# Performance work log

Measured on AMD Instinct MI355X. Metric: run time of the kernel, lower is better.

The kernel has to match this reference:

```python
import jax, jax.numpy as jnp
import numpy as np

B, S, D, H = 2, 2048, 1024, 16
DH = D // H
CBS, STRIDE = 32, 16      # compress block size / sliding stride
NSEL = 16                 # num_selected_blocks
WIN = 16                  # sliding_window_size (half-width)
SCALE = DH ** -0.5


def setup_inputs() -> dict:
    key = jax.random.key(0)
    ks = jax.random.split(key, 12)
    s = 0.02
    return {
        "x": jax.random.normal(ks[0], (B, S, D), jnp.float32),
        "qkv_w": jax.random.normal(ks[1], (D, 3 * D), jnp.float32) * s,
        "qkv_b": jnp.zeros((3 * D,), jnp.float32),
        "c1_w": jax.random.normal(ks[2], (CBS * D, D), jnp.float32) * s,
        "c1_b": jnp.zeros((D,), jnp.float32),
        "c2_w": jax.random.normal(ks[3], (D, D), jnp.float32) * s,
        "c2_b": jnp.zeros((D,), jnp.float32),
        "score_w": jax.random.normal(ks[4], (D, 1), jnp.float32) * s,
        "score_b": jnp.zeros((1,), jnp.float32),
        "out_w": jax.random.normal(ks[5], (D, D), jnp.float32) * s,
        "out_b": jnp.zeros((D,), jnp.float32),
    }


def reference(x, qkv_w, qkv_b, c1_w, c1_b, c2_w, c2_b, score_w, score_b, out_w, out_b):
    # q, k, v: [B, H, S, DH]
    qkv = (x @ qkv_w + qkv_b).reshape(B, S, 3, H, DH).transpose(2, 0, 3, 1, 4)
    q, k, v = qkv[0], qkv[1], qkv[2]

    # --- token compression: overlapping blocks -> MLP ---
    starts = jnp.arange(0, S - CBS + 1, STRIDE)                 # [nb]
    blk_idx = starts[:, None] + jnp.arange(CBS)[None, :]        # [nb, CBS]
    blocks = x[:, blk_idx, :].reshape(B, starts.shape[0], CBS * D)
    hidden = jax.nn.relu(blocks @ c1_w + c1_b)
    compressed = hidden @ c2_w + c2_b                           # [B, nb, D]

    # --- block selection via learned scores + top-k ---
    scores = (compressed @ score_w + score_b)[..., 0]           # [B, nb]
    _, top_idx = jax.lax.top_k(scores, NSEL)                    # [B, NSEL]
    selected = jnp.take_along_axis(compressed, top_idx[:, :, None], axis=1)  # [B, NSEL, D]

    sqkv = (selected @ qkv_w + qkv_b).reshape(B, NSEL, 3, H, DH).transpose(2, 0, 3, 1, 4)
    sel_k, sel_v = sqkv[1], sqkv[2]                             # [B, H, NSEL, DH]

    # --- sliding-window local attention (vectorized gather of banded K/V) ---
    offs = jnp.arange(-WIN, WIN + 1)                            # [2W+1]
    pos = jnp.arange(S)[:, None] + offs[None, :]                # [S, 2W+1]
    valid = (pos >= 0) & (pos < S)
    pos_c = jnp.clip(pos, 0, S - 1)
    kw = k[:, :, pos_c, :]                                      # [B, H, S, 2W+1, DH]
    vw = v[:, :, pos_c, :]
    sc = jnp.einsum('bhsd,bhswd->bhsw', q, kw) * SCALE
    sc = jnp.where(valid[None, None], sc, -jnp.inf)
    local = jnp.einsum('bhsw,bhswd->bhsd', jax.nn.softmax(sc, axis=-1), vw)

    # --- global attention over selected compressed blocks ---
    gsc = jnp.einsum('bhsd,bhkd->bhsk', q, sel_k) * SCALE       # [B, H, S, NSEL]
    glob = jnp.einsum('bhsk,bhkd->bhsd', jax.nn.softmax(gsc, axis=-1), sel_v)

    out = (local + glob).transpose(0, 2, 1, 3).reshape(B, S, D)
    return out @ out_w + out_b
```

## Files before the change

### kernel.cpp

```cpp
#include <hip/hip_runtime.h>
#include <math.h>

#define BB   2
#define SS   2048
#define DD   1024
#define HH   16
#define DH   64
#define CBS  32
#define STRIDEC 16
#define NBLK 127
#define NSEL 16
#define WIN  16
#define NW   33
#define SCALE 0.125f
#define MC   254

typedef _Float16 f16;
typedef __attribute__((ext_vector_type(8))) _Float16 f16x8;
typedef __attribute__((ext_vector_type(4))) _Float16 f16x4;
typedef __attribute__((ext_vector_type(2))) _Float16 h2;
typedef __attribute__((ext_vector_type(4))) float f32x4;

__global__ __launch_bounds__(256) void convert_f16(
    const float* __restrict__ src, f16* __restrict__ dst, int n)
{
    const int i = (blockIdx.x * 256 + threadIdx.x) * 4;
    if (i >= n) return;
    float4 v = *(const float4*)(src + i);
    f16x4 o;
    o[0] = (f16)v.x; o[1] = (f16)v.y; o[2] = (f16)v.z; o[3] = (f16)v.w;
    *(f16x4*)(dst + i) = o;
}

__global__ __launch_bounds__(256) void transpose_conv(
    const float* __restrict__ src, f16* __restrict__ dst, int K, int N)
{
    __shared__ float t[32][33];
    const int n0 = blockIdx.x * 32, k0 = blockIdx.y * 32;
    const int tx = threadIdx.x & 31, ty = threadIdx.x >> 5;
#pragma unroll
    for (int r = 0; r < 32; r += 8)
        t[ty + r][tx] = src[(size_t)(k0 + ty + r) * N + n0 + tx];
    __syncthreads();
#pragma unroll
    for (int r = 0; r < 32; r += 8)
        dst[(size_t)(n0 + ty + r) * K + k0 + tx] = (f16)t[tx][ty + r];
}

__global__ __launch_bounds__(256) void gemm_f16(
    const f16* __restrict__ A, const f16* __restrict__ Bt,
    const float* __restrict__ bias, float* __restrict__ C,
    int M, int N, int K)
{
    constexpr int BK = 64;
    __shared__ f16 As[128 * BK];
    __shared__ f16 Bs[128 * BK];
    const int tid  = threadIdx.x;
    const int wid  = tid >> 6, lane = tid & 63;
    const int bm = blockIdx.y * 128, bn = blockIdx.x * 128;
    const int wm = (wid >> 1) * 64, wn = (wid & 1) * 64;

    const int lrow = lane >> 3;
    const int lk8  = (lane & 7) * 8;

    f32x4 acc[4][4];
#pragma unroll
    for (int i = 0; i < 4; ++i)
#pragma unroll
        for (int j = 0; j < 4; ++j) acc[i][j] = (f32x4){0.f, 0.f, 0.f, 0.f};

    for (int kt = 0; kt < K; kt += BK) {
#pragma unroll
        for (int c = 0; c < 4; ++c) {
            const int seg = c * 4 + wid;
            const int row = seg * 8 + lrow;
            const f16* ga = A + (size_t)(bm + row) * K + kt + lk8;
            __builtin_amdgcn_global_load_lds(
                (const __attribute__((address_space(1))) void*)(const void*)ga,
                (__attribute__((address_space(3))) void*)(void*)(As + seg * 512),
                16, 0, 0);
            const f16* gb = Bt + (size_t)(bn + row) * K + kt + lk8;
            __builtin_amdgcn_global_load_lds(
                (const __attribute__((address_space(1))) void*)(const void*)gb,
                (__attribute__((address_space(3))) void*)(void*)(Bs + seg * 512),
                16, 0, 0);
        }
        __syncthreads();

#pragma unroll
        for (int kk = 0; kk < 2; ++kk) {
            const int ko = kk * 32 + (lane >> 4) * 8;
            f16x8 a[4], b[4];
#pragma unroll
            for (int i = 0; i < 4; ++i)
                a[i] = *(const f16x8*)(As + (wm + i * 16 + (lane & 15)) * BK + ko);
#pragma unroll
            for (int j = 0; j < 4; ++j)
                b[j] = *(const f16x8*)(Bs + (wn + j * 16 + (lane & 15)) * BK + ko);
#pragma unroll
            for (int i = 0; i < 4; ++i)
#pragma unroll
                for (int j = 0; j < 4; ++j)
                    acc[i][j] = __builtin_amdgcn_mfma_f32_16x16x32_f16(
                        a[i], b[j], acc[i][j], 0, 0, 0);
        }
        __syncthreads();
    }

    const int rr0 = (lane >> 4) * 4;
    const int cc  = lane & 15;
#pragma unroll
    for (int i = 0; i < 4; ++i) {
        const int r = bm + wm + i * 16 + rr0;
#pragma unroll
        for (int j = 0; j < 4; ++j) {
            const int cn = bn + wn + j * 16 + cc;
            const float bv = bias[cn];
#pragma unroll
            for (int q = 0; q < 4; ++q)
                C[(size_t)(r + q) * N + cn] = acc[i][j][q] + bv;
        }
    }
}

#define C1_NZ 16
#define C1_KCHUNK 2048

__global__ __launch_bounds__(256) void gemm_c1(
    const f16* __restrict__ xh, const f16* __restrict__ Wt,
    float* __restrict__ P)
{
    constexpr int BK = 64;
    __shared__ f16 As[128 * BK];
    __shared__ f16 Bs[64 * BK];
    const int tid  = threadIdx.x;
    const int wid  = tid >> 6, lane = tid & 63;
    const int bn = blockIdx.x * 64, bm = blockIdx.y * 128;
    const int z  = blockIdx.z;
    const int wm = (wid >> 1) * 64, wn = (wid & 1) * 32;

    const int lrow = lane >> 3;
    const int lk8  = (lane & 7) * 8;

    f32x4 acc[4][2];
#pragma unroll
    for (int i = 0; i < 4; ++i)
#pragma unroll
        for (int j = 0; j < 2; ++j) acc[i][j] = (f32x4){0.f, 0.f, 0.f, 0.f};

    for (int t = 0; t < C1_KCHUNK / BK; ++t) {
        const int ktg = z * C1_KCHUNK + t * BK;
        const int kc  = (ktg + lk8) >> 10;
        const int kd  = (ktg + lk8) & 1023;
#pragma unroll
        for (int c = 0; c < 4; ++c) {
            const int seg = c * 4 + wid;
            int row = bm + seg * 8 + lrow;
            if (row > MC - 1) row = MC - 1;
            const int b   = (row >= NBLK) ? 1 : 0;
            const int blk = row - b * NBLK;
            const f16* ga = xh + ((size_t)(b * SS + blk * STRIDEC + kc) << 10) + kd;
            __builtin_amdgcn_global_load_lds(
                (const __attribute__((address_space(1))) void*)(const void*)ga,
                (__attribute__((address_space(3))) void*)(void*)(As + seg * 512),
                16, 0, 0);
        }
#pragma unroll
        for (int c = 0; c < 2; ++c) {
            const int seg = wid * 2 + c;
            const int row = bn + seg * 8 + lrow;
            const f16* gb = Wt + (size_t)row * (CBS * DD) + ktg + lk8;
            __builtin_amdgcn_global_load_lds(
                (const __attribute__((address_space(1))) void*)(const void*)gb,
                (__attribute__((address_space(3))) void*)(void*)(Bs + seg * 512),
                16, 0, 0);
        }
        __syncthreads();

#pragma unroll
        for (int kk = 0; kk < 2; ++kk) {
            const int ko = kk * 32 + (lane >> 4) * 8;
            f16x8 a[4], b[2];
#pragma unroll
            for (int i = 0; i < 4; ++i)
                a[i] = *(const f16x8*)(As + (wm + i * 16 + (lane & 15)) * BK + ko);
#pragma unroll
            for (int j = 0; j < 2; ++j)
                b[j] = *(const f16x8*)(Bs + (wn + j * 16 + (lane & 15)) * BK + ko);
#pragma unroll
            for (int i = 0; i < 4; ++i)
#pragma unroll
                for (int j = 0; j < 2; ++j)
                    acc[i][j] = __builtin_amdgcn_mfma_f32_16x16x32_f16(
                        a[i], b[j], acc[i][j], 0, 0, 0);
        }
        __syncthreads();
    }

    const int rr0 = (lane >> 4) * 4;
    const int cc  = lane & 15;
#pragma unroll
    for (int i = 0; i < 4; ++i) {
        const int r = bm + wm + i * 16 + rr0;
#pragma unroll
        for (int j = 0; j < 2; ++j) {
            const int cn = bn + wn + j * 16 + cc;
#pragma unroll
            for (int q = 0; q < 4; ++q)
                if (r + q < MC)
                    P[((size_t)z * MC + r + q) * DD + cn] = acc[i][j][q];
        }
    }
}

template<int MODE>
__global__ __launch_bounds__(256) void gemm128(
    const float* __restrict__ A, const float* __restrict__ Bm,
    const float* __restrict__ bias, float* __restrict__ C,
    int M, int N, int K, const int* __restrict__ selIdx, int flags)
{
    __shared__ float As[8][132];
    __shared__ float Bs[8][132];

    const int tid = threadIdx.x;
    const int bm = blockIdx.y * 128;
    const int bn = blockIdx.x * 128;
    const int nz = gridDim.z;
    const int z  = blockIdx.z;
    const int kchunk = K / nz;
    const int k0 = z * kchunk;
    const int kend = k0 + kchunk;

    const int tx = tid & 15;
    const int ty = tid >> 4;

    const int arow = tid >> 1;
    const int akq  = (tid & 1) * 4;
    const int bkr  = tid >> 5;
    const int bcol = (tid & 31) * 4;

    float acc[2][2][4][4];
#pragma unroll
    for (int qi = 0; qi < 2; ++qi)
#pragma unroll
        for (int qj = 0; qj < 2; ++qj)
#pragma unroll
            for (int i = 0; i < 4; ++i)
#pragma unroll
                for (int j = 0; j < 4; ++j) acc[qi][qj][i][j] = 0.f;

    auto loadA = [&](int kt) -> float4 {
        float4 av = make_float4(0.f, 0.f, 0.f, 0.f);
        const int grow = bm + arow;
        if (grow < M) {
            if constexpr (MODE == 0) {
                av = *(const float4*)(A + (size_t)grow * K + kt + akq);
            } else {
                const int b = grow >> 4;
                const int j = grow & 15;
                const int idx = selIdx[b * NSEL + j];
                av = *(const float4*)(A + (size_t)(b * NBLK + idx) * K + kt + akq);
            }
        }
        return av;
    };
    auto loadB = [&](int kt) -> float4 {
        return *(const float4*)(Bm + (size_t)(kt + bkr) * N + bn + bcol);
    };

    float4 av = loadA(k0);
    float4 bv = loadB(k0);

    for (int kt = k0; kt < kend; kt += 8) {
        As[akq + 0][arow] = av.x;
        As[akq + 1][arow] = av.y;
        As[akq + 2][arow] = av.z;
        As[akq + 3][arow] = av.w;
        *(float4*)&Bs[bkr][bcol] = bv;
        __syncthreads();
        if (kt + 8 < kend) {
            av = loadA(kt + 8);
            bv = loadB(kt + 8);
        }
#pragma unroll
        for (int k = 0; k < 8; ++k) {
            const float4 a0 = *(const float4*)&As[k][ty * 4];
            const float4 a1 = *(const float4*)&As[k][64 + ty * 4];
            const float4 b0 = *(const float4*)&Bs[k][tx * 4];
            const float4 b1 = *(const float4*)&Bs[k][64 + tx * 4];
            const float ar[2][4] = {{a0.x, a0.y, a0.z, a0.w},
                                    {a1.x, a1.y, a1.z, a1.w}};
            const float br[2][4] = {{b0.x, b0.y, b0.z, b0.w},
                                    {b1.x, b1.y, b1.z, b1.w}};
#pragma unroll
            for (int qi = 0; qi < 2; ++qi)
#pragma unroll
                for (int i = 0; i < 4; ++i)
#pragma unroll
                    for (int qj = 0; qj < 2; ++qj)
#pragma unroll
                        for (int j = 0; j < 4; ++j)
                            acc[qi][qj][i][j] += ar[qi][i] * br[qj][j];
        }
        __syncthreads();
    }

    if (nz == 1) {
        const bool hasB   = (flags & 1) != 0;
        const bool doRelu = (flags & 2) != 0;
#pragma unroll
        for (int qi = 0; qi < 2; ++qi)
#pragma unroll
            for (int i = 0; i < 4; ++i) {
                const int r = bm + qi * 64 + ty * 4 + i;
                if (r >= M) continue;
#pragma unroll
                for (int qj = 0; qj < 2; ++qj)
#pragma unroll
                    for (int j = 0; j < 4; ++j) {
                        const int cn = bn + qj * 64 + tx * 4 + j;
                        float v = acc[qi][qj][i][j];
                        if (hasB) v += bias[cn];
                        if (doRelu) v = fmaxf(v, 0.f);
                        C[(size_t)r * N + cn] = v;
                    }
            }
    } else {
        float* P = C + (size_t)z * M * N;
#pragma unroll
        for (int qi = 0; qi < 2; ++qi)
#pragma unroll
            for (int i = 0; i < 4; ++i) {
                const int r = bm + qi * 64 + ty * 4 + i;
                if (r >= M) continue;
#pragma unroll
                for (int qj = 0; qj < 2; ++qj)
#pragma unroll
                    for (int j = 0; j < 4; ++j) {
                        const int cn = bn + qj * 64 + tx * 4 + j;
                        P[(size_t)r * N + cn] = acc[qi][qj][i][j];
                    }
            }
    }
}

__global__ __launch_bounds__(256) void reduce_partials(
    const float* __restrict__ P, const float* __restrict__ bias,
    float* __restrict__ outp, int MN, int N, int nz, int doRelu)
{
    const int i = blockIdx.x * 256 + threadIdx.x;
    if (i >= MN) return;
    float s = 0.f;
    for (int z = 0; z < nz; ++z) s += P[(size_t)z * MN + i];
    s += bias[i % N];
    if (doRelu) s = fmaxf(s, 0.f);
    outp[i] = s;
}

__global__ __launch_bounds__(256) void score_kernel(
    const float* __restrict__ comp, const float* __restrict__ sw,
    const float* __restrict__ sb, float* __restrict__ scores)
{
    const int row = blockIdx.x;
    const float* cp = comp + (size_t)row * DD;
    float s = 0.f;
    for (int k = threadIdx.x; k < DD; k += 256) s += cp[k] * sw[k];
#pragma unroll
    for (int off = 32; off >= 1; off >>= 1) s += __shfl_xor(s, off);
    __shared__ float red[4];
    if ((threadIdx.x & 63) == 0) red[threadIdx.x >> 6] = s;
    __syncthreads();
    if (threadIdx.x == 0) scores[row] = red[0] + red[1] + red[2] + red[3] + sb[0];
}

__global__ __launch_bounds__(128) void topk_kernel(
    const float* __restrict__ scores, int* __restrict__ top)
{
    const int b = blockIdx.x;
    const int t = threadIdx.x;
    __shared__ float sval[128];
    __shared__ float sv2[128];
    __shared__ int   si2[128];
    __shared__ unsigned char used[128];
    sval[t] = (t < NBLK) ? scores[b * NBLK + t] : -INFINITY;
    used[t] = 0;
    __syncthreads();
    for (int j = 0; j < NSEL; ++j) {
        sv2[t] = used[t] ? -INFINITY : sval[t];
        si2[t] = t;
        __syncthreads();
        for (int stp = 64; stp >= 1; stp >>= 1) {
            if (t < stp) {
                if (sv2[t + stp] > sv2[t] ||
                    (sv2[t + stp] == sv2[t] && si2[t + stp] < si2[t])) {
                    sv2[t] = sv2[t + stp];
                    si2[t] = si2[t + stp];
                }
            }
            __syncthreads();
        }
        if (t == 0) { top[b * NSEL + j] = si2[0]; used[si2[0]] = 1; }
        __syncthreads();
    }
}

#define QT 64
#define KROWS 96
#define KST2 72
#define VST 136
#define PST 136

__global__ __launch_bounds__(256) void attn_mfma(
    const float* __restrict__ qkv, const float* __restrict__ sqkv,
    f16* __restrict__ attn)
{
    __shared__ f16 Kl[KROWS][KST2];
    __shared__ f16 sKl[NSEL][KST2];
    __shared__ f16 Vt[DH][VST];
    __shared__ f16 Pl[4][16][PST];

    int bid = blockIdx.x;
    bid = (bid & 7) * (gridDim.x >> 3) + (bid >> 3);
    const int t = bid & 31;
    const int h = (bid >> 5) & (HH - 1);
    const int b = bid >> 9;
    const int s0 = t * QT;

    const int tid = threadIdx.x;
    const int wid = tid >> 6, lane = tid & 63;
    const int l15 = lane & 15, lg = lane >> 4;

    for (int i = tid; i < KROWS * 16; i += 256) {
        const int row = i >> 4, c4 = (i & 15) * 4;
        const int pos = s0 - WIN + row;
        float4 kv = make_float4(0.f, 0.f, 0.f, 0.f), vv = kv;
        if (pos >= 0 && pos < SS) {
            const float* base = qkv + (size_t)(b * SS + pos) * (3 * DD) + h * DH + c4;
            kv = *(const float4*)(base + DD);
            vv = *(const float4*)(base + 2 * DD);
        }
        f16x4 kh;
        kh[0] = (f16)kv.x; kh[1] = (f16)kv.y; kh[2] = (f16)kv.z; kh[3] = (f16)kv.w;
        *(f16x4*)&Kl[row][c4] = kh;
        Vt[c4 + 0][row] = (f16)vv.x; Vt[c4 + 1][row] = (f16)vv.y;
        Vt[c4 + 2][row] = (f16)vv.z; Vt[c4 + 3][row] = (f16)vv.w;
    }
    {
        const int si = tid >> 4, c4 = (tid & 15) * 4;
        const float* base = sqkv + (size_t)(b * NSEL + si) * (3 * DD) + h * DH + c4;
        float4 kv = *(const float4*)(base + DD);
        float4 vv = *(const float4*)(base + 2 * DD);
        f16x4 kh;
        kh[0] = (f16)kv.x; kh[1] = (f16)kv.y; kh[2] = (f16)kv.z; kh[3] = (f16)kv.w;
        *(f16x4*)&sKl[si][c4] = kh;
        Vt[c4 + 0][96 + si] = (f16)vv.x; Vt[c4 + 1][96 + si] = (f16)vv.y;
        Vt[c4 + 2][96 + si] = (f16)vv.z; Vt[c4 + 3][96 + si] = (f16)vv.w;
    }
    for (int i = tid; i < DH * 16; i += 256)
        Vt[i >> 4][112 + (i & 15)] = (f16)0.f;

    f16x8 qf[2];
    {
        const float* qp = qkv + (size_t)(b * SS + s0 + wid * 16 + l15) * (3 * DD)
                        + h * DH + lg * 8;
#pragma unroll
        for (int kc = 0; kc < 2; ++kc) {
            float4 va = *(const float4*)(qp + kc * 32);
            float4 vb = *(const float4*)(qp + kc * 32 + 4);
            f16x8 q;
            q[0] = (f16)va.x; q[1] = (f16)va.y; q[2] = (f16)va.z; q[3] = (f16)va.w;
            q[4] = (f16)vb.x; q[5] = (f16)vb.y; q[6] = (f16)vb.z; q[7] = (f16)vb.w;
            qf[kc] = q;
        }
    }
    __syncthreads();

    f32x4 aqk[6], asel;
#pragma unroll
    for (int i = 0; i < 6; ++i) aqk[i] = (f32x4){0.f, 0.f, 0.f, 0.f};
    asel = (f32x4){0.f, 0.f, 0.f, 0.f};
#pragma unroll
    for (int kc = 0; kc < 2; ++kc) {
        const int ko = kc * 32 + lg * 8;
#pragma unroll
        for (int kvb = 0; kvb < 6; ++kvb) {
            f16x8 ka = *(const f16x8*)&Kl[kvb * 16 + l15][ko];
            aqk[kvb] = __builtin_amdgcn_mfma_f32_16x16x32_f16(ka, qf[kc], aqk[kvb], 0, 0, 0);
        }
        f16x8 ks = *(const f16x8*)&sKl[l15][ko];
        asel = __builtin_amdgcn_mfma_f32_16x16x32_f16(ks, qf[kc], asel, 0, 0, 0);
    }

    const int qt_ = wid * 16 + l15;
    float sc[6][4];
    float m = -INFINITY;
#pragma unroll
    for (int kvb = 0; kvb < 6; ++kvb)
#pragma unroll
        for (int r = 0; r < 4; ++r) {
            const int kv  = kvb * 16 + lg * 4 + r;
            const int pos = s0 - WIN + kv;
            const int dlt = kv - qt_;
            const bool ok = (dlt >= 0) & (dlt <= 32) & (pos >= 0) & (pos < SS);
            sc[kvb][r] = ok ? aqk[kvb][r] * SCALE : -INFINITY;
            m = fmaxf(m, sc[kvb][r]);
        }
    m = fmaxf(m, __shfl_xor(m, 16));
    m = fmaxf(m, __shfl_xor(m, 32));
    float sum = 0.f;
#pragma unroll
    for (int kvb = 0; kvb < 6; ++kvb)
#pragma unroll
        for (int r = 0; r < 4; ++r) {
            sc[kvb][r] = __expf(sc[kvb][r] - m);
            sum += sc[kvb][r];
        }
    sum += __shfl_xor(sum, 16);
    sum += __shfl_xor(sum, 32);
    const float inv1 = 1.f / sum;

    float s2[4];
    float m2 = -INFINITY;
#pragma unroll
    for (int r = 0; r < 4; ++r) { s2[r] = asel[r] * SCALE; m2 = fmaxf(m2, s2[r]); }
    m2 = fmaxf(m2, __shfl_xor(m2, 16));
    m2 = fmaxf(m2, __shfl_xor(m2, 32));
    float sum2 = 0.f;
#pragma unroll
    for (int r = 0; r < 4; ++r) { s2[r] = __expf(s2[r] - m2); sum2 += s2[r]; }
    sum2 += __shfl_xor(sum2, 16);
    sum2 += __shfl_xor(sum2, 32);
    const float inv2 = 1.f / sum2;

#pragma unroll
    for (int kvb = 0; kvb < 6; ++kvb) {
        h2 p01, p23;
        p01[0] = (f16)(sc[kvb][0] * inv1); p01[1] = (f16)(sc[kvb][1] * inv1);
        p23[0] = (f16)(sc[kvb][2] * inv1); p23[1] = (f16)(sc[kvb][3] * inv1);
        *(h2*)&Pl[wid][l15][kvb * 16 + lg * 4]     = p01;
        *(h2*)&Pl[wid][l15][kvb * 16 + lg * 4 + 2] = p23;
    }
    {
        h2 g01, g23, z0;
        g01[0] = (f16)(s2[0] * inv2); g01[1] = (f16)(s2[1] * inv2);
        g23[0] = (f16)(s2[2] * inv2); g23[1] = (f16)(s2[3] * inv2);
        z0[0] = (f16)0.f; z0[1] = (f16)0.f;
        *(h2*)&Pl[wid][l15][96 + lg * 4]      = g01;
        *(h2*)&Pl[wid][l15][96 + lg * 4 + 2]  = g23;
        *(h2*)&Pl[wid][l15][112 + lg * 4]     = z0;
        *(h2*)&Pl[wid][l15][112 + lg * 4 + 2] = z0;
    }
    __syncthreads();

    f32x4 ov[4];
#pragma unroll
    for (int i = 0; i < 4; ++i) ov[i] = (f32x4){0.f, 0.f, 0.f, 0.f};
#pragma unroll
    for (int kc = 0; kc < 4; ++kc) {
        const int ko = kc * 32 + lg * 8;
        f16x8 pa = *(const f16x8*)&Pl[wid][l15][ko];
#pragma unroll
        for (int db = 0; db < 4; ++db) {
            f16x8 vb = *(const f16x8*)&Vt[db * 16 + l15][ko];
            ov[db] = __builtin_amdgcn_mfma_f32_16x16x32_f16(pa, vb, ov[db], 0, 0, 0);
        }
    }

    const size_t rbase = (size_t)(b * SS + s0 + wid * 16 + lg * 4);
#pragma unroll
    for (int r = 0; r < 4; ++r) {
        f16* op = attn + (rbase + r) * DD + h * DH + l15;
#pragma unroll
        for (int db = 0; db < 4; ++db)
            op[db * 16] = (f16)ov[db][r];
    }
}

extern "C" void kernel_launch(void* const* d_in, const int* in_sizes, int n_in,
                              void* d_out, int out_size, void* d_ws, size_t ws_size,
                              hipStream_t stream)
{
    const float* x       = (const float*)d_in[0];
    const float* qkv_w   = (const float*)d_in[1];
    const float* qkv_b   = (const float*)d_in[2];
    const float* c1_w    = (const float*)d_in[3];
    const float* c1_b    = (const float*)d_in[4];
    const float* c2_w    = (const float*)d_in[5];
    const float* c2_b    = (const float*)d_in[6];
    const float* score_w = (const float*)d_in[7];
    const float* score_b = (const float*)d_in[8];
    const float* out_w   = (const float*)d_in[9];
    const float* out_b   = (const float*)d_in[10];
    float* out = (float*)d_out;
    float* ws  = (float*)d_ws;

    f16*   xh     = (f16*)ws;
    float* A1     = ws + 2097152;
    f16*   WTc1   = (f16*)A1;
    float* qkvb   = A1;
    f16*   attnf  = (f16*)(A1 + 12582912);
    float* A2     = ws + 18874368;
    float* part   = A2;
    f16*   qkv_wT = (f16*)A2;
    f16*   out_wT = (f16*)(A2 + 1572864);
    float* hidden = ws + 23035904;
    float* comp   = hidden + 260096;
    float* scores = comp + 260096;
    int*   topIdx = (int*)(scores + 256);
    float* sqkvb  = scores + 256 + 64;

    const int MROWS = BB * SS;
    const int MSEL  = BB * NSEL;

    convert_f16<<<(MROWS * DD) / (256 * 4), 256, 0, stream>>>(x, xh, MROWS * DD);

    transpose_conv<<<dim3(DD / 32, CBS * DD / 32), 256, 0, stream>>>(
        c1_w, WTc1, CBS * DD, DD);

    gemm_c1<<<dim3(DD / 64, 2, C1_NZ), 256, 0, stream>>>(xh, WTc1, part);

    reduce_partials<<<(MC * DD) / 256, 256, 0, stream>>>(
        part, c1_b, hidden, MC * DD, DD, C1_NZ, 1);

    gemm128<0><<<dim3(DD / 128, 2, 16), 256, 0, stream>>>(
        hidden, c2_w, nullptr, part, MC, DD, DD, nullptr, 0);

    reduce_partials<<<(MC * DD) / 256, 256, 0, stream>>>(
        part, c2_b, comp, MC * DD, DD, 16, 0);

    score_kernel<<<MC, 256, 0, stream>>>(comp, score_w, score_b, scores);

    topk_kernel<<<BB, 128, 0, stream>>>(scores, topIdx);

    gemm128<2><<<dim3(3 * DD / 128, 1, 16), 256, 0, stream>>>(
        comp, qkv_w, nullptr, part, MSEL, 3 * DD, DD, topIdx, 0);

    reduce_partials<<<(MSEL * 3 * DD + 255) / 256, 256, 0, stream>>>(
        part, qkv_b, sqkvb, MSEL * 3 * DD, 3 * DD, 16, 0);

    transpose_conv<<<dim3(3 * DD / 32, DD / 32), 256, 0, stream>>>(
        qkv_w, qkv_wT, DD, 3 * DD);
    transpose_conv<<<dim3(DD / 32, DD / 32), 256, 0, stream>>>(
        out_w, out_wT, DD, DD);

    gemm_f16<<<dim3(3 * DD / 128, MROWS / 128), 256, 0, stream>>>(
        xh, qkv_wT, qkv_b, qkvb, MROWS, 3 * DD, DD);

    attn_mfma<<<BB * HH * (SS / QT), 256, 0, stream>>>(qkvb, sqkvb, attnf);

    gemm_f16<<<dim3(DD / 128, MROWS / 128), 256, 0, stream>>>(
        attnf, out_wT, out_b, out, MROWS, DD, DD);
}
```

Measured before the change: 258.4 us.

## Fuse c1 weight conversion into GEMM loader and emit f16 QKV for attention

Drops the separate transpose/convert pass over the large c1 weight: gemm_c1 now reads fp32 weights directly, converts them to f16 and stores them into a padded, swizzled shared tile. The QKV projection and the selected-block QKV reduction now write f16, so the attention kernel loads half-width data without converting, and one block barrier is removed. This cuts a full write-and-reread of the weight and halves QKV traffic, but the GEMM now does scalar conversions and shared stores in its inner loop, and f16 storage of QKV reduces precision.

```diff
diff --git a/kernel.cpp b/kernel.cpp
--- a/kernel.cpp
+++ b/kernel.cpp
@@ -47,6 +47,7 @@
         dst[(size_t)(n0 + ty + r) * K + k0 + tx] = (f16)t[tx][ty + r];
 }
 
+template<int OUT16>
 __global__ __launch_bounds__(256) void gemm_f16(
     const f16* __restrict__ A, const f16* __restrict__ Bt,
     const float* __restrict__ bias, float* __restrict__ C,
@@ -117,8 +118,12 @@
             const int cn = bn + wn + j * 16 + cc;
             const float bv = bias[cn];
 #pragma unroll
-            for (int q = 0; q < 4; ++q)
-                C[(size_t)(r + q) * N + cn] = acc[i][j][q] + bv;
+            for (int q = 0; q < 4; ++q) {
+                if constexpr (OUT16)
+                    ((f16*)C)[(size_t)(r + q) * N + cn] = (f16)(acc[i][j][q] + bv);
+                else
+                    C[(size_t)(r + q) * N + cn] = acc[i][j][q] + bv;
+            }
         }
     }
 }
@@ -127,12 +132,13 @@
 #define C1_KCHUNK 2048
 
 __global__ __launch_bounds__(256) void gemm_c1(
-    const f16* __restrict__ xh, const f16* __restrict__ Wt,
+    const f16* __restrict__ xh, const float* __restrict__ c1w,
     float* __restrict__ P)
 {
     constexpr int BK = 64;
+    constexpr int BSTR = 72;
     __shared__ f16 As[128 * BK];
-    __shared__ f16 Bs[64 * BK];
+    __shared__ f16 Bs[64 * BSTR];
     const int tid  = threadIdx.x;
     const int wid  = tid >> 6, lane = tid & 63;
     const int bn = blockIdx.x * 64, bm = blockIdx.y * 128;
@@ -165,15 +171,24 @@
                 (__attribute__((address_space(3))) void*)(void*)(As + seg * 512),
                 16, 0, 0);
         }
-#pragma unroll
-        for (int c = 0; c < 2; ++c) {
-            const int seg = wid * 2 + c;
-            const int row = bn + seg * 8 + lrow;
-            const f16* gb = Wt + (size_t)row * (CBS * DD) + ktg + lk8;
-            __builtin_amdgcn_global_load_lds(
-                (const __attribute__((address_space(1))) void*)(const void*)gb,
-                (__attribute__((address_space(3))) void*)(void*)(Bs + seg * 512),
-                16, 0, 0);
+        {
+            const int kk0 = (tid >> 4) * 2;
+            const int n4  = (tid & 15) * 4;
+#pragma unroll
+            for (int p = 0; p < 2; ++p) {
+                const int kk = kk0 + p * 32;
+                const float* gB = c1w + (size_t)(ktg + kk) * DD + bn + n4;
+                float4 r0 = *(const float4*)gB;
+                float4 r1 = *(const float4*)(gB + DD);
+                const float a0[4] = {r0.x, r0.y, r0.z, r0.w};
+                const float a1[4] = {r1.x, r1.y, r1.z, r1.w};
+#pragma unroll
+                for (int u = 0; u < 4; ++u) {
+                    const int n = n4 + u;
+                    h2 w; w[0] = (f16)a0[u]; w[1] = (f16)a1[u];
+                    *(h2*)&Bs[n * BSTR + (kk ^ (((n >> 3) & 3) << 3))] = w;
+                }
+            }
         }
         __syncthreads();
 
@@ -185,8 +200,10 @@
             for (int i = 0; i < 4; ++i)
                 a[i] = *(const f16x8*)(As + (wm + i * 16 + (lane & 15)) * BK + ko);
 #pragma unroll
-            for (int j = 0; j < 2; ++j)
-                b[j] = *(const f16x8*)(Bs + (wn + j * 16 + (lane & 15)) * BK + ko);
+            for (int j = 0; j < 2; ++j) {
+                const int n = wn + j * 16 + (lane & 15);
+                b[j] = *(const f16x8*)&Bs[n * BSTR + (ko ^ (((n >> 3) & 3) << 3))];
+            }
 #pragma unroll
             for (int i = 0; i < 4; ++i)
 #pragma unroll
@@ -346,7 +363,7 @@
 
 __global__ __launch_bounds__(256) void reduce_partials(
     const float* __restrict__ P, const float* __restrict__ bias,
-    float* __restrict__ outp, int MN, int N, int nz, int doRelu)
+    float* __restrict__ outp, int MN, int N, int nz, int doRelu, int halfOut)
 {
     const int i = blockIdx.x * 256 + threadIdx.x;
     if (i >= MN) return;
@@ -354,7 +371,8 @@
     for (int z = 0; z < nz; ++z) s += P[(size_t)z * MN + i];
     s += bias[i % N];
     if (doRelu) s = fmaxf(s, 0.f);
-    outp[i] = s;
+    if (halfOut) ((f16*)outp)[i] = (f16)s;
+    else         outp[i] = s;
 }
 
 __global__ __launch_bounds__(256) void score_kernel(
@@ -411,7 +429,7 @@
 #define PST 136
 
 __global__ __launch_bounds__(256) void attn_mfma(
-    const float* __restrict__ qkv, const float* __restrict__ sqkv,
+    const f16* __restrict__ qkv, const f16* __restrict__ sqkv,
     f16* __restrict__ attn)
 {
     __shared__ f16 Kl[KROWS][KST2];
@@ -430,48 +448,39 @@
     const int wid = tid >> 6, lane = tid & 63;
     const int l15 = lane & 15, lg = lane >> 4;
 
-    for (int i = tid; i < KROWS * 16; i += 256) {
-        const int row = i >> 4, c4 = (i & 15) * 4;
+    for (int i = tid; i < KROWS * 8; i += 256) {
+        const int row = i >> 3, c8 = (i & 7) * 8;
         const int pos = s0 - WIN + row;
-        float4 kv = make_float4(0.f, 0.f, 0.f, 0.f), vv = kv;
+        f16x8 kv, vv;
+#pragma unroll
+        for (int u = 0; u < 8; ++u) { kv[u] = (f16)0.f; vv[u] = (f16)0.f; }
         if (pos >= 0 && pos < SS) {
-            const float* base = qkv + (size_t)(b * SS + pos) * (3 * DD) + h * DH + c4;
-            kv = *(const float4*)(base + DD);
-            vv = *(const float4*)(base + 2 * DD);
-        }
-        f16x4 kh;
-        kh[0] = (f16)kv.x; kh[1] = (f16)kv.y; kh[2] = (f16)kv.z; kh[3] = (f16)kv.w;
-        *(f16x4*)&Kl[row][c4] = kh;
-        Vt[c4 + 0][row] = (f16)vv.x; Vt[c4 + 1][row] = (f16)vv.y;
-        Vt[c4 + 2][row] = (f16)vv.z; Vt[c4 + 3][row] = (f16)vv.w;
-    }
-    {
-        const int si = tid >> 4, c4 = (tid & 15) * 4;
-        const float* base = sqkv + (size_t)(b * NSEL + si) * (3 * DD) + h * DH + c4;
-        float4 kv = *(const float4*)(base + DD);
-        float4 vv = *(const float4*)(base + 2 * DD);
-        f16x4 kh;
-        kh[0] = (f16)kv.x; kh[1] = (f16)kv.y; kh[2] = (f16)kv.z; kh[3] = (f16)kv.w;
-        *(f16x4*)&sKl[si][c4] = kh;
-        Vt[c4 + 0][96 + si] = (f16)vv.x; Vt[c4 + 1][96 + si] = (f16)vv.y;
-        Vt[c4 + 2][96 + si] = (f16)vv.z; Vt[c4 + 3][96 + si] = (f16)vv.w;
+            const f16* base = qkv + (size_t)(b * SS + pos) * (3 * DD) + h * DH + c8;
+            kv = *(const f16x8*)(base + DD);
+            vv = *(const f16x8*)(base + 2 * DD);
+        }
+        *(f16x8*)&Kl[row][c8] = kv;
+#pragma unroll
+        for (int u = 0; u < 8; ++u) Vt[c8 + u][row] = vv[u];
+    }
+    if (tid < NSEL * 8) {
+        const int si = tid >> 3, c8 = (tid & 7) * 8;
+        const f16* base = sqkv + (size_t)(b * NSEL + si) * (3 * DD) + h * DH + c8;
+        f16x8 kv = *(const f16x8*)(base + DD);
+        f16x8 vv = *(const f16x8*)(base + 2 * DD);
+        *(f16x8*)&sKl[si][c8] = kv;
+#pragma unroll
+        for (int u = 0; u < 8; ++u) Vt[c8 + u][96 + si] = vv[u];
     }
     for (int i = tid; i < DH * 16; i += 256)
         Vt[i >> 4][112 + (i & 15)] = (f16)0.f;
 
     f16x8 qf[2];
     {
-        const float* qp = qkv + (size_t)(b * SS + s0 + wid * 16 + l15) * (3 * DD)
-                        + h * DH + lg * 8;
-#pragma unroll
-        for (int kc = 0; kc < 2; ++kc) {
-            float4 va = *(const float4*)(qp + kc * 32);
-            float4 vb = *(const float4*)(qp + kc * 32 + 4);
-            f16x8 q;
-            q[0] = (f16)va.x; q[1] = (f16)va.y; q[2] = (f16)va.z; q[3] = (f16)va.w;
-            q[4] = (f16)vb.x; q[5] = (f16)vb.y; q[6] = (f16)vb.z; q[7] = (f16)vb.w;
-            qf[kc] = q;
-        }
+        const f16* qp = qkv + (size_t)(b * SS + s0 + wid * 16 + l15) * (3 * DD)
+                      + h * DH + lg * 8;
+        qf[0] = *(const f16x8*)(qp);
+        qf[1] = *(const f16x8*)(qp + 32);
     }
     __syncthreads();
 
@@ -550,7 +559,6 @@
         *(h2*)&Pl[wid][l15][112 + lg * 4]     = z0;
         *(h2*)&Pl[wid][l15][112 + lg * 4 + 2] = z0;
     }
-    __syncthreads();
 
     f32x4 ov[4];
 #pragma unroll
@@ -596,8 +604,7 @@
 
     f16*   xh     = (f16*)ws;
     float* A1     = ws + 2097152;
-    f16*   WTc1   = (f16*)A1;
-    float* qkvb   = A1;
+    f16*   qkvb   = (f16*)A1;
     f16*   attnf  = (f16*)(A1 + 12582912);
     float* A2     = ws + 18874368;
     float* part   = A2;
@@ -614,19 +621,16 @@
 
     convert_f16<<<(MROWS * DD) / (256 * 4), 256, 0, stream>>>(x, xh, MROWS * DD);
 
-    transpose_conv<<<dim3(DD / 32, CBS * DD / 32), 256, 0, stream>>>(
-        c1_w, WTc1, CBS * DD, DD);
-
-    gemm_c1<<<dim3(DD / 64, 2, C1_NZ), 256, 0, stream>>>(xh, WTc1, part);
+    gemm_c1<<<dim3(DD / 64, 2, C1_NZ), 256, 0, stream>>>(xh, c1_w, part);
 
     reduce_partials<<<(MC * DD) / 256, 256, 0, stream>>>(
-        part, c1_b, hidden, MC * DD, DD, C1_NZ, 1);
+        part, c1_b, hidden, MC * DD, DD, C1_NZ, 1, 0);
 
     gemm128<0><<<dim3(DD / 128, 2, 16), 256, 0, stream>>>(
         hidden, c2_w, nullptr, part, MC, DD, DD, nullptr, 0);
 
     reduce_partials<<<(MC * DD) / 256, 256, 0, stream>>>(
-        part, c2_b, comp, MC * DD, DD, 16, 0);
+        part, c2_b, comp, MC * DD, DD, 16, 0, 0);
 
     score_kernel<<<MC, 256, 0, stream>>>(comp, score_w, score_b, scores);
 
@@ -636,18 +640,19 @@
         comp, qkv_w, nullptr, part, MSEL, 3 * DD, DD, topIdx, 0);
 
     reduce_partials<<<(MSEL * 3 * DD + 255) / 256, 256, 0, stream>>>(
-        part, qkv_b, sqkvb, MSEL * 3 * DD, 3 * DD, 16, 0);
+        part, qkv_b, sqkvb, MSEL * 3 * DD, 3 * DD, 16, 0, 1);
 
     transpose_conv<<<dim3(3 * DD / 32, DD / 32), 256, 0, stream>>>(
         qkv_w, qkv_wT, DD, 3 * DD);
     transpose_conv<<<dim3(DD / 32, DD / 32), 256, 0, stream>>>(
         out_w, out_wT, DD, DD);
 
-    gemm_f16<<<dim3(3 * DD / 128, MROWS / 128), 256, 0, stream>>>(
-        xh, qkv_wT, qkv_b, qkvb, MROWS, 3 * DD, DD);
-
-    attn_mfma<<<BB * HH * (SS / QT), 256, 0, stream>>>(qkvb, sqkvb, attnf);
-
-    gemm_f16<<<dim3(DD / 128, MROWS / 128), 256, 0, stream>>>(
+    gemm_f16<1><<<dim3(3 * DD / 128, MROWS / 128), 256, 0, stream>>>(
+        xh, qkv_wT, qkv_b, (float*)qkvb, MROWS, 3 * DD, DD);
+
+    attn_mfma<<<BB * HH * (SS / QT), 256, 0, stream>>>(
+        qkvb, (const f16*)sqkvb, attnf);
+
+    gemm_f16<0><<<dim3(DD / 128, MROWS / 128), 256, 0, stream>>>(
         attnf, out_wT, out_b, out, MROWS, DD, DD);
 }
```

After: 220.0 us. 1.17x faster.
